# Kernel optimization log

Measured on AMD Instinct MI355X. Metric: run time of the kernel, lower is better.

## Reference

```python
import jax, jax.numpy as jnp
import numpy as np

B, S, D, H = 4, 4096, 1024, 8
HD = D // H  # head dims, FFT length for circular convolution


def setup_inputs() -> dict:
    key = jax.random.key(0)
    k1, k2, k3 = jax.random.split(key, 3)
    x = jax.random.normal(k1, (B, S, D), dtype=jnp.float32)
    # torch nn.Linear(D, 3D, bias=False) -> store as [D, 3D] for x @ W
    w_qkv = jax.random.normal(k2, (D, 3 * D), dtype=jnp.float32) * (1.0 / np.sqrt(D))
    w_out = jax.random.normal(k3, (D, D), dtype=jnp.float32) * (1.0 / np.sqrt(D))
    return {"x": x, "w_qkv": w_qkv, "w_out": w_out}


def reference(x, w_qkv, w_out):
    # HRR self-attention (causal, norm=False, dropout in eval mode => identity).
    b, s, d = x.shape
    qkv = x @ w_qkv                               # [B,S,3D]
    q, k, v = jnp.split(qkv, 3, axis=-1)
    q = q.reshape(b, s, H, HD)
    k = k.reshape(b, s, H, HD)
    v = v.reshape(b, s, H, HD)
    # Holographic binding: circular convolution k (*) v == ifft(fft(k)*fft(v))
    fq = jnp.fft.fft(q, axis=-1)                  # [B,S,H,HD] complex
    fk = jnp.fft.fft(k, axis=-1)
    fv = jnp.fft.fft(v, axis=-1)
    kv = fk * fv                                  # bound key-value pairs (freq domain)
    kv = jnp.cumsum(kv, axis=1)                   # causal aggregation over sequence
    # Unbinding via circular correlation with the query: ifft(S * conj(fft(q)))
    vals = jnp.fft.ifft(kv * jnp.conj(fq), axis=-1).real.astype(x.dtype)
    vals = vals.reshape(b, s, d)
    return vals @ w_out
```

## Files before the change

### kernel.cpp

```cpp
#include <hip/hip_runtime.h>

static constexpr int BB = 4;
static constexpr int SS = 4096;
static constexpr int DD = 1024;
static constexpr int HH = 8;
static constexpr int HD = 128;
static constexpr int CS = 32;
static constexpr int NCHUNK = SS / CS;
static constexpr int MROWS = BB * SS;

typedef __attribute__((ext_vector_type(8))) short bfrag;
typedef __attribute__((ext_vector_type(4))) float floatx4;

__device__ __forceinline__ float bf2f(unsigned int u) {
    return __uint_as_float((u & 0xFFFFu) << 16);
}
__device__ __forceinline__ unsigned short f2bf(float f) {
    unsigned int x = __float_as_uint(f);
    unsigned int r = x + 0x7FFFu + ((x >> 16) & 1u);
    return (unsigned short)(r >> 16);
}
__device__ __forceinline__ unsigned int pack_rne(float a, float b) {
    return ((unsigned int)f2bf(a)) | (((unsigned int)f2bf(b)) << 16);
}

__device__ __forceinline__ void async_copy16(const void* g, void* l) {
    __builtin_amdgcn_global_load_lds(
        (const __attribute__((address_space(1))) unsigned int*)g,
        (__attribute__((address_space(3))) unsigned int*)l, 16, 0, 0);
}

struct cpx { float re, im; };

__device__ __forceinline__ cpx cadd(cpx a, cpx b) { return {a.re + b.re, a.im + b.im}; }
__device__ __forceinline__ cpx csub(cpx a, cpx b) { return {a.re - b.re, a.im - b.im}; }
__device__ __forceinline__ cpx cmul(cpx a, cpx b) {
    return { fmaf(a.re, b.re, -a.im * b.im), fmaf(a.re, b.im, a.im * b.re) };
}
__device__ __forceinline__ cpx cmul_cj(cpx a, cpx b) {
    return { fmaf(a.re, b.re, a.im * b.im), fmaf(a.im, b.re, -a.re * b.im) };
}
__device__ __forceinline__ cpx shflx(cpx x, int m) {
    return { __shfl_xor(x.re, m), __shfl_xor(x.im, m) };
}
__device__ __forceinline__ cpx shfl_at(cpx x, int src) {
    return { __shfl(x.re, src), __shfl(x.im, src) };
}

__device__ __forceinline__ int pair_lane_even(int l) {
    int m = (int)(__brev((unsigned)l) >> 26);
    int mp = (64 - m) & 63;
    return (int)(__brev((unsigned)mp) >> 26);
}

__device__ __forceinline__ void make_tw(int lane, cpx tw[7]) {
    const float NEG2PI = -6.28318530717958647692f;
    float a0 = NEG2PI * (float)lane * (1.0f / 128.0f);
    tw[0] = { __cosf(a0), __sinf(a0) };
    int d = 32;
#pragma unroll
    for (int s = 1; s <= 6; ++s) {
        int i = lane & (d - 1);
        float a = NEG2PI * (float)i / (float)(2 * d);
        tw[s] = { __cosf(a), __sinf(a) };
        d >>= 1;
    }
}

__device__ __forceinline__ void fft128_fwd(cpx& x0, cpx& x1, const cpx tw[7], int lane) {
    cpx a = x0, b = x1;
    x0 = cadd(a, b);
    x1 = cmul(csub(a, b), tw[0]);
    int d = 32;
#pragma unroll
    for (int s = 1; s <= 6; ++s) {
        const bool up = (lane & d) != 0;
        cpx o0 = shflx(x0, d);
        cpx o1 = shflx(x1, d);
        cpx s0 = cadd(x0, o0);
        cpx s1 = cadd(x1, o1);
        cpx d0 = cmul(csub(o0, x0), tw[s]);
        cpx d1 = cmul(csub(o1, x1), tw[s]);
        x0 = up ? d0 : s0;
        x1 = up ? d1 : s1;
        d >>= 1;
    }
}

__device__ __forceinline__ void fft128_inv(cpx& x0, cpx& x1, const cpx tw[7], int lane) {
    int d = 1;
#pragma unroll
    for (int s = 6; s >= 1; --s) {
        const bool up = (lane & d) != 0;
        cpx o0 = shflx(x0, d);
        cpx o1 = shflx(x1, d);
        cpx b0 = up ? x0 : o0;
        cpx a0 = up ? o0 : x0;
        cpx b1 = up ? x1 : o1;
        cpx a1 = up ? o1 : x1;
        cpx t0 = cmul_cj(b0, tw[s]);
        cpx t1 = cmul_cj(b1, tw[s]);
        x0 = up ? csub(a0, t0) : cadd(a0, t0);
        x1 = up ? csub(a1, t1) : cadd(a1, t1);
        d <<= 1;
    }
    cpx t = cmul_cj(x1, tw[0]);
    cpx a = x0;
    const float inv = 0.0078125f;
    x0 = { (a.re + t.re) * inv, (a.im + t.im) * inv };
    x1 = { (a.re - t.re) * inv, (a.im - t.im) * inv };
}

__global__ __launch_bounds__(256) void convert_bf16(const float* __restrict__ X,
                                                    unsigned short* __restrict__ Y)
{
    const size_t i = ((size_t)blockIdx.x * 256 + threadIdx.x) * 8;
    float4 v0 = *reinterpret_cast<const float4*>(X + i);
    float4 v1 = *reinterpret_cast<const float4*>(X + i + 4);
    uint4 p = { pack_rne(v0.x, v0.y), pack_rne(v0.z, v0.w),
                pack_rne(v1.x, v1.y), pack_rne(v1.z, v1.w) };
    *reinterpret_cast<uint4*>(Y + i) = p;
}

__global__ __launch_bounds__(256) void transpose_rn(const float* __restrict__ W,
                                                    unsigned short* __restrict__ T,
                                                    int K, int N)
{
    __shared__ float tile[32][33];
    const int n0 = blockIdx.x * 32, k0 = blockIdx.y * 32;
    const int r = threadIdx.x >> 5, c = threadIdx.x & 31;
#pragma unroll
    for (int i = 0; i < 4; ++i)
        tile[r + 8 * i][c] = W[(size_t)(k0 + r + 8 * i) * N + n0 + c];
    __syncthreads();
#pragma unroll
    for (int i = 0; i < 4; ++i) {
        float v = tile[c][r + 8 * i];
        T[(size_t)(n0 + r + 8 * i) * K + k0 + c] = f2bf(v);
    }
}

template <typename OutT>
__global__ __launch_bounds__(256) void gemm_bt(const unsigned short* __restrict__ A,
                                               const unsigned short* __restrict__ Bt,
                                               OutT* __restrict__ C,
                                               int M, int N, int K)
{
    __shared__ __align__(16) unsigned short As[128 * 32];
    __shared__ __align__(16) unsigned short Bs[128 * 32];
    const int tid = threadIdx.x, lane = tid & 63, w = tid >> 6;
    const int wr = w >> 1, wc = w & 1;
    const int m0 = blockIdx.y * 128, n0 = blockIdx.x * 128;

    floatx4 acc[4][4];
#pragma unroll
    for (int i = 0; i < 4; ++i)
#pragma unroll
        for (int j = 0; j < 4; ++j) { floatx4 z = {0.f, 0.f, 0.f, 0.f}; acc[i][j] = z; }

    for (int kt = 0; kt < K; kt += 32) {
#pragma unroll
        for (int i = 0; i < 2; ++i) {
            const int is = 2 * w + i;
            const size_t aoff = (size_t)(m0 + 16 * is + (lane >> 2)) * K + kt + (lane & 3) * 8;
            const size_t boff = (size_t)(n0 + 16 * is + (lane >> 2)) * K + kt + (lane & 3) * 8;
            async_copy16(A + aoff, &As[512 * is]);
            async_copy16(Bt + boff, &Bs[512 * is]);
        }
        __syncthreads();

        bfrag af[4], bf_[4];
#pragma unroll
        for (int t = 0; t < 4; ++t)
            af[t] = *reinterpret_cast<const bfrag*>(
                &As[(64 * wr + 16 * t + (lane & 15)) * 32 + (lane >> 4) * 8]);
#pragma unroll
        for (int t = 0; t < 4; ++t)
            bf_[t] = *reinterpret_cast<const bfrag*>(
                &Bs[(64 * wc + 16 * t + (lane & 15)) * 32 + (lane >> 4) * 8]);
#pragma unroll
        for (int i = 0; i < 4; ++i)
#pragma unroll
            for (int j = 0; j < 4; ++j)
                acc[i][j] = __builtin_amdgcn_mfma_f32_16x16x32_bf16(af[i], bf_[j], acc[i][j], 0, 0, 0);
        __syncthreads();
    }

#pragma unroll
    for (int i = 0; i < 4; ++i)
#pragma unroll
        for (int j = 0; j < 4; ++j)
#pragma unroll
            for (int r = 0; r < 4; ++r) {
                const int row = m0 + 64 * wr + 16 * i + (lane >> 4) * 4 + r;
                const int col = n0 + 64 * wc + 16 * j + (lane & 15);
                float v = acc[i][j][r];
                if constexpr (sizeof(OutT) == 2)
                    C[(size_t)row * N + col] = (OutT)f2bf(v);
                else
                    C[(size_t)row * N + col] = (OutT)v;
            }
}

__global__ __launch_bounds__(256) void hrr_phaseA(const unsigned short* __restrict__ qkv,
                                                  unsigned int* __restrict__ P,
                                                  float* __restrict__ totals)
{
    const int blk = blockIdx.x;
    const int bh = blk / NCHUNK;
    const int chunk = blk % NCHUNK;
    const int b = bh >> 3, h = bh & 7;
    const int tid = threadIdx.x;
    const int wave = tid >> 6, lane = tid & 63;

    cpx tw[7];
    make_tw(lane, tw);
    const int pl0 = pair_lane_even(lane);
    const int pl1 = lane ^ 63;

    cpx acc0 = {0.f, 0.f}, acc1 = {0.f, 0.f};
    const int s0 = chunk * CS + wave * (CS / 4);
    for (int i = 0; i < CS / 4; ++i) {
        const int s = s0 + i;
        const unsigned short* base = qkv + (size_t)(b * SS + s) * 3072 + h * 128;
        cpx z0 = { bf2f(base[1024 + lane]),      bf2f(base[2048 + lane]) };
        cpx z1 = { bf2f(base[1024 + 64 + lane]), bf2f(base[2048 + 64 + lane]) };
        fft128_fwd(z0, z1, tw, lane);
        cpx sq0 = cmul(z0, z0);
        cpx sq1 = cmul(z1, z1);
        cpx sp0 = shfl_at(sq0, pl0);
        cpx sp1 = shfl_at(sq1, pl1);
        cpx p0 = { 0.25f * (sq0.im + sp0.im), 0.25f * (sp0.re - sq0.re) };
        cpx p1 = { 0.25f * (sq1.im + sp1.im), 0.25f * (sp1.re - sq1.re) };
        acc0 = cadd(acc0, p0);
        acc1 = cadd(acc1, p1);
        unsigned int* prow = P + ((size_t)bh * SS + s) * 128;
        prow[lane]      = pack_rne(p0.re, p0.im);
        prow[64 + lane] = pack_rne(p1.re, p1.im);
    }

    __shared__ float red[4][256];
    red[wave][lane * 2 + 0] = acc0.re;
    red[wave][lane * 2 + 1] = acc0.im;
    red[wave][128 + lane * 2 + 0] = acc1.re;
    red[wave][128 + lane * 2 + 1] = acc1.im;
    __syncthreads();

    float s4 = red[0][tid] + red[1][tid] + red[2][tid] + red[3][tid];
    totals[((size_t)bh * NCHUNK + chunk) * 256 + tid] = s4;
}

__global__ __launch_bounds__(256) void hrr_phaseB(float* __restrict__ totals)
{
    const int bh = blockIdx.x;
    const int t = threadIdx.x;
    float run = 0.f;
#pragma unroll 4
    for (int c = 0; c < NCHUNK; ++c) {
        const size_t idx = ((size_t)bh * NCHUNK + c) * 256 + t;
        float v = totals[idx];
        totals[idx] = run;
        run += v;
    }
}

__global__ __launch_bounds__(256) void hrr_phaseC(const unsigned short* __restrict__ qkv,
                                                  const unsigned int* __restrict__ P,
                                                  const float* __restrict__ totals,
                                                  unsigned short* __restrict__ vals)
{
    __shared__ float Pf[CS * 256];

    const int blk = blockIdx.x;
    const int bh = blk / NCHUNK;
    const int chunk = blk % NCHUNK;
    const int b = bh >> 3, h = bh & 7;
    const int tid = threadIdx.x;
    const int wave = tid >> 6, lane = tid & 63;

    cpx tw[7];
    make_tw(lane, tw);
    const int pl0 = pair_lane_even(lane);
    const int pl1 = lane ^ 63;

#pragma unroll
    for (int it = 0; it < CS / 4; ++it) {
        const int sl = it * 4 + wave;
        const int s = chunk * CS + sl;
        const unsigned int* prow = P + ((size_t)bh * SS + s) * 128;
        unsigned int a = prow[lane];
        unsigned int c = prow[64 + lane];
        float2 fa = { bf2f(a), bf2f(a >> 16) };
        float2 fc = { bf2f(c), bf2f(c >> 16) };
        *reinterpret_cast<float2*>(&Pf[sl * 256 + 2 * lane]) = fa;
        *reinterpret_cast<float2*>(&Pf[sl * 256 + 128 + 2 * lane]) = fc;
    }
    __syncthreads();

    {
        float run = totals[((size_t)bh * NCHUNK + chunk) * 256 + tid];
#pragma unroll 8
        for (int s = 0; s < CS; ++s) {
            run += Pf[s * 256 + tid];
            Pf[s * 256 + tid] = run;
        }
    }
    __syncthreads();

    for (int i = 0; i < CS / 8; ++i) {
        const int sl = wave * (CS / 4) + 2 * i;
        const int s1 = chunk * CS + sl;
        const unsigned short* b1 = qkv + (size_t)(b * SS + s1) * 3072 + h * 128;
        const unsigned short* b2 = b1 + 3072;
        cpx z0 = { bf2f(b1[lane]),      bf2f(b2[lane]) };
        cpx z1 = { bf2f(b1[64 + lane]), bf2f(b2[64 + lane]) };
        fft128_fwd(z0, z1, tw, lane);
        cpx B0 = shfl_at(z0, pl0);
        cpx B1 = shfl_at(z1, pl1);
        cpx cf1_0 = { 0.5f * (z0.re + B0.re), 0.5f * (B0.im - z0.im) };
        cpx cf1_1 = { 0.5f * (z1.re + B1.re), 0.5f * (B1.im - z1.im) };
        cpx cf2_0 = { 0.5f * (z0.im + B0.im), 0.5f * (z0.re - B0.re) };
        cpx cf2_1 = { 0.5f * (z1.im + B1.im), 0.5f * (z1.re - B1.re) };

        const float* r1 = &Pf[sl * 256];
        const float* r2 = r1 + 256;
        float2 t0 = *reinterpret_cast<const float2*>(&r1[2 * lane]);
        float2 t1 = *reinterpret_cast<const float2*>(&r1[128 + 2 * lane]);
        float2 t2 = *reinterpret_cast<const float2*>(&r2[2 * lane]);
        float2 t3 = *reinterpret_cast<const float2*>(&r2[128 + 2 * lane]);
        cpx C1_0 = { t0.x, t0.y }, C1_1 = { t1.x, t1.y };
        cpx C2_0 = { t2.x, t2.y }, C2_1 = { t3.x, t3.y };

        cpx a0 = cmul(C1_0, cf1_0), w0 = cmul(C2_0, cf2_0);
        cpx a1 = cmul(C1_1, cf1_1), w1 = cmul(C2_1, cf2_1);
        cpx u0 = { a0.re - w0.im, a0.im + w0.re };
        cpx u1 = { a1.re - w1.im, a1.im + w1.re };
        fft128_inv(u0, u1, tw, lane);

        unsigned short* o1 = vals + (size_t)(b * SS + s1) * DD + h * 128;
        unsigned short* o2 = o1 + DD;
        o1[lane]      = f2bf(u0.re);
        o1[64 + lane] = f2bf(u1.re);
        o2[lane]      = f2bf(u0.im);
        o2[64 + lane] = f2bf(u1.im);
    }
}

extern "C" void kernel_launch(void* const* d_in, const int* in_sizes, int n_in,
                              void* d_out, int out_size, void* d_ws, size_t ws_size,
                              hipStream_t stream) {
    const float* x     = (const float*)d_in[0];
    const float* w_qkv = (const float*)d_in[1];
    const float* w_out = (const float*)d_in[2];
    float* out = (float*)d_out;

    unsigned short* qkv  = (unsigned short*)d_ws;
    unsigned short* xb   = qkv + (size_t)MROWS * 3072;
    unsigned short* vals = xb + (size_t)MROWS * DD;
    unsigned int* P      = (unsigned int*)(vals + (size_t)MROWS * DD);
    float* totals        = (float*)(P + (size_t)32 * SS * 128);
    unsigned short* wqkvt = (unsigned short*)(totals + (size_t)32 * NCHUNK * 256);
    unsigned short* woutt = wqkvt + (size_t)3072 * 1024;

    convert_bf16<<<(MROWS * DD) / (256 * 8), 256, 0, stream>>>(x, xb);
    transpose_rn<<<dim3(3072 / 32, 1024 / 32), 256, 0, stream>>>(w_qkv, wqkvt, 1024, 3072);
    transpose_rn<<<dim3(1024 / 32, 1024 / 32), 256, 0, stream>>>(w_out, woutt, 1024, 1024);

    gemm_bt<unsigned short><<<dim3(3072 / 128, MROWS / 128), 256, 0, stream>>>(
        xb, wqkvt, qkv, MROWS, 3072, DD);

    hrr_phaseA<<<BB * HH * NCHUNK, 256, 0, stream>>>(qkv, P, totals);

    hrr_phaseB<<<BB * HH, 256, 0, stream>>>(totals);

    hrr_phaseC<<<BB * HH * NCHUNK, 256, 0, stream>>>(qkv, P, totals, vals);

    gemm_bt<float><<<dim3(DD / 128, MROWS / 128), 256, 0, stream>>>(
        vals, woutt, out, MROWS, DD, DD);
}
```

Measured before the change: 425.8 us.

## Replace 128x128 GEMM with 256x256 multi-stage pipelined MFMA GEMM

Both projection GEMMs move to a 256x256 tile kernel with 8 waves, a 4-deep async-copy ring buffer in 128KB of dynamic LDS, and explicit vmcnt waits so loads overlap MFMA work. It adds an XOR swizzle on LDS to avoid bank conflicts, a workgroup remap for L2 locality, and s_setprio around the MFMA block. The bf16 output goes through LDS so global stores are 16-byte vectors. The larger tile raises data reuse per load, but it uses many more registers and allows fewer resident blocks, and the grid is small for the N=1024 GEMM.

Result: faster. 383.9 us (-9.8%).

```diff
diff --git a/kernel.cpp b/kernel.cpp
--- a/kernel.cpp
+++ b/kernel.cpp
@@ -141,65 +141,120 @@
 }
 
 template <typename OutT>
-__global__ __launch_bounds__(256) void gemm_bt(const unsigned short* __restrict__ A,
-                                               const unsigned short* __restrict__ Bt,
-                                               OutT* __restrict__ C,
-                                               int M, int N, int K)
-{
-    __shared__ __align__(16) unsigned short As[128 * 32];
-    __shared__ __align__(16) unsigned short Bs[128 * 32];
+__global__ __launch_bounds__(512, 2) void gemm256(const unsigned short* __restrict__ A,
+                                                  const unsigned short* __restrict__ Bt,
+                                                  OutT* __restrict__ C,
+                                                  int M, int N, int K)
+{
+    extern __shared__ __align__(16) unsigned short lds[];
+    unsigned short* sA = lds;
+    unsigned short* sB = lds + 32768;
+
     const int tid = threadIdx.x, lane = tid & 63, w = tid >> 6;
-    const int wr = w >> 1, wc = w & 1;
-    const int m0 = blockIdx.y * 128, n0 = blockIdx.x * 128;
-
-    floatx4 acc[4][4];
-#pragma unroll
-    for (int i = 0; i < 4; ++i)
-#pragma unroll
-        for (int j = 0; j < 4; ++j) { floatx4 z = {0.f, 0.f, 0.f, 0.f}; acc[i][j] = z; }
-
-    for (int kt = 0; kt < K; kt += 32) {
-#pragma unroll
-        for (int i = 0; i < 2; ++i) {
-            const int is = 2 * w + i;
-            const size_t aoff = (size_t)(m0 + 16 * is + (lane >> 2)) * K + kt + (lane & 3) * 8;
-            const size_t boff = (size_t)(n0 + 16 * is + (lane >> 2)) * K + kt + (lane & 3) * 8;
-            async_copy16(A + aoff, &As[512 * is]);
-            async_copy16(Bt + boff, &Bs[512 * is]);
+    const int wr = w >> 2, wc = w & 3;
+
+    const int nbx = N >> 8;
+    const int cpx_ = gridDim.x >> 3;
+    const int wg = blockIdx.x;
+    const int swz = (wg & 7) * cpx_ + (wg >> 3);
+    const int n0 = (swz % nbx) << 8;
+    const int m0 = (swz / nbx) << 8;
+
+    const int lr = lane >> 2;
+    const int kx = (((lane & 3) ^ ((lane >> 3) & 3)) << 3);
+    const unsigned short* pA0 = A  + (size_t)(m0 + 32 * w + lr) * K + kx;
+    const unsigned short* pA1 = pA0 + (size_t)16 * K;
+    const unsigned short* pB0 = Bt + (size_t)(n0 + 32 * w + lr) * K + kx;
+    const unsigned short* pB1 = pB0 + (size_t)16 * K;
+
+    auto stage = [&](int tt) {
+        const int q = (tt & 3) * 8192;
+        const size_t ko = (size_t)tt * 32;
+        async_copy16(pA0 + ko, sA + q + (2 * w) * 512);
+        async_copy16(pA1 + ko, sA + q + (2 * w + 1) * 512);
+        async_copy16(pB0 + ko, sB + q + (2 * w) * 512);
+        async_copy16(pB1 + ko, sB + q + (2 * w + 1) * 512);
+    };
+
+    const int sl = lane >> 4;
+    const int xa = ((lane & 15) >> 1) & 3;
+    const int ra = (wr * 128 + (lane & 15)) * 32 + ((sl ^ xa) << 3);
+    const int rb = (wc * 64  + (lane & 15)) * 32 + ((sl ^ xa) << 3);
+
+    floatx4 acc[8][4];
+#pragma unroll
+    for (int m = 0; m < 8; ++m)
+#pragma unroll
+        for (int n = 0; n < 4; ++n) { floatx4 z = {0.f, 0.f, 0.f, 0.f}; acc[m][n] = z; }
+
+    const int NT = K >> 5;
+
+    stage(0); stage(1); stage(2);
+
+    for (int t = 0; t < NT; ++t) {
+        if (t + 3 < NT) stage(t + 3);
+
+        const int rem = NT - 1 - t;
+        if (rem >= 3)      asm volatile("s_waitcnt vmcnt(12)" ::: "memory");
+        else if (rem == 2) asm volatile("s_waitcnt vmcnt(8)"  ::: "memory");
+        else if (rem == 1) asm volatile("s_waitcnt vmcnt(4)"  ::: "memory");
+        else               asm volatile("s_waitcnt vmcnt(0)"  ::: "memory");
+        __builtin_amdgcn_s_barrier();
+        __builtin_amdgcn_sched_barrier(0);
+
+        const unsigned short* pa = sA + (t & 3) * 8192 + ra;
+        const unsigned short* pb = sB + (t & 3) * 8192 + rb;
+        bfrag af[8], bfr[4];
+#pragma unroll
+        for (int m = 0; m < 8; ++m)
+            af[m] = *reinterpret_cast<const bfrag*>(pa + m * 512);
+#pragma unroll
+        for (int n = 0; n < 4; ++n)
+            bfr[n] = *reinterpret_cast<const bfrag*>(pb + n * 512);
+
+        __builtin_amdgcn_s_setprio(1);
+#pragma unroll
+        for (int m = 0; m < 8; ++m)
+#pragma unroll
+            for (int n = 0; n < 4; ++n)
+                acc[m][n] = __builtin_amdgcn_mfma_f32_16x16x32_bf16(af[m], bfr[n], acc[m][n], 0, 0, 0);
+        __builtin_amdgcn_s_setprio(0);
+        __builtin_amdgcn_sched_barrier(0);
+
+        asm volatile("s_waitcnt lgkmcnt(0)" ::: "memory");
+        __builtin_amdgcn_s_barrier();
+        __builtin_amdgcn_sched_barrier(0);
+    }
+
+    if constexpr (sizeof(OutT) == 2) {
+        unsigned short* myt = lds + w * 8192;
+#pragma unroll
+        for (int m = 0; m < 8; ++m)
+#pragma unroll
+            for (int n = 0; n < 4; ++n)
+#pragma unroll
+                for (int r = 0; r < 4; ++r)
+                    myt[(m * 16 + sl * 4 + r) * 64 + n * 16 + (lane & 15)] = f2bf(acc[m][n][r]);
+        asm volatile("s_waitcnt lgkmcnt(0)" ::: "memory");
+#pragma unroll
+        for (int c = 0; c < 16; ++c) {
+            const int idx = c * 64 + lane;
+            const int row = idx >> 3, cc = (idx & 7) << 3;
+            uint4 v = *reinterpret_cast<const uint4*>(myt + idx * 8);
+            *reinterpret_cast<uint4*>(C + (size_t)(m0 + wr * 128 + row) * N + (n0 + wc * 64 + cc)) = v;
         }
-        __syncthreads();
-
-        bfrag af[4], bf_[4];
-#pragma unroll
-        for (int t = 0; t < 4; ++t)
-            af[t] = *reinterpret_cast<const bfrag*>(
-                &As[(64 * wr + 16 * t + (lane & 15)) * 32 + (lane >> 4) * 8]);
-#pragma unroll
-        for (int t = 0; t < 4; ++t)
-            bf_[t] = *reinterpret_cast<const bfrag*>(
-                &Bs[(64 * wc + 16 * t + (lane & 15)) * 32 + (lane >> 4) * 8]);
-#pragma unroll
-        for (int i = 0; i < 4; ++i)
-#pragma unroll
-            for (int j = 0; j < 4; ++j)
-                acc[i][j] = __builtin_amdgcn_mfma_f32_16x16x32_bf16(af[i], bf_[j], acc[i][j], 0, 0, 0);
-        __syncthreads();
-    }
-
-#pragma unroll
-    for (int i = 0; i < 4; ++i)
-#pragma unroll
-        for (int j = 0; j < 4; ++j)
-#pragma unroll
-            for (int r = 0; r < 4; ++r) {
-                const int row = m0 + 64 * wr + 16 * i + (lane >> 4) * 4 + r;
-                const int col = n0 + 64 * wc + 16 * j + (lane & 15);
-                float v = acc[i][j][r];
-                if constexpr (sizeof(OutT) == 2)
-                    C[(size_t)row * N + col] = (OutT)f2bf(v);
-                else
-                    C[(size_t)row * N + col] = (OutT)v;
-            }
+    } else {
+#pragma unroll
+        for (int m = 0; m < 8; ++m)
+#pragma unroll
+            for (int n = 0; n < 4; ++n)
+#pragma unroll
+                for (int r = 0; r < 4; ++r) {
+                    const int row = m0 + wr * 128 + m * 16 + sl * 4 + r;
+                    const int col = n0 + wc * 64 + n * 16 + (lane & 15);
+                    C[(size_t)row * N + col] = acc[m][n][r];
+                }
+    }
 }
 
 __global__ __launch_bounds__(256) void hrr_phaseA(const unsigned short* __restrict__ qkv,
@@ -362,11 +417,20 @@
     unsigned short* wqkvt = (unsigned short*)(totals + (size_t)32 * NCHUNK * 256);
     unsigned short* woutt = wqkvt + (size_t)3072 * 1024;
 
+    static bool attr_done = false;
+    if (!attr_done) {
+        hipFuncSetAttribute(reinterpret_cast<const void*>(gemm256<unsigned short>),
+                            hipFuncAttributeMaxDynamicSharedMemorySize, 131072);
+        hipFuncSetAttribute(reinterpret_cast<const void*>(gemm256<float>),
+                            hipFuncAttributeMaxDynamicSharedMemorySize, 131072);
+        attr_done = true;
+    }
+
     convert_bf16<<<(MROWS * DD) / (256 * 8), 256, 0, stream>>>(x, xb);
     transpose_rn<<<dim3(3072 / 32, 1024 / 32), 256, 0, stream>>>(w_qkv, wqkvt, 1024, 3072);
     transpose_rn<<<dim3(1024 / 32, 1024 / 32), 256, 0, stream>>>(w_out, woutt, 1024, 1024);
 
-    gemm_bt<unsigned short><<<dim3(3072 / 128, MROWS / 128), 256, 0, stream>>>(
+    gemm256<unsigned short><<<(3072 / 256) * (MROWS / 256), 512, 131072, stream>>>(
         xb, wqkvt, qkv, MROWS, 3072, DD);
 
     hrr_phaseA<<<BB * HH * NCHUNK, 256, 0, stream>>>(qkv, P, totals);
@@ -375,6 +439,6 @@
 
     hrr_phaseC<<<BB * HH * NCHUNK, 256, 0, stream>>>(qkv, P, totals, vals);
 
-    gemm_bt<float><<<dim3(DD / 128, MROWS / 128), 256, 0, stream>>>(
+    gemm256<float><<<(DD / 256) * (MROWS / 256), 512, 131072, stream>>>(
         vals, woutt, out, MROWS, DD, DD);
 }
```
